# Kernel optimization log

Measured on AMD Instinct MI355X. Metric: run time of the kernel, lower is better.

Reference implementation:

```python
import jax, jax.numpy as jnp
import numpy as np

B, N, H = 8192, 8, 1024  # batch, DOF, hidden width; state dim = 2*N


def setup_inputs() -> dict:
    key = jax.random.key(0)
    ks = jax.random.split(key, 4)
    s1 = 1.0 / np.sqrt(2 * N)
    s2 = 1.0 / np.sqrt(H)
    return {
        "x": jax.random.normal(ks[0], (B, 2 * N), dtype=jnp.float32),
        "W1": jax.random.normal(ks[1], (2 * N, H), dtype=jnp.float32) * s1,
        "b1": jnp.zeros((H,), dtype=jnp.float32),
        "W2": jax.random.normal(ks[2], (H, H), dtype=jnp.float32) * s2,
        "b2": jnp.zeros((H,), dtype=jnp.float32),
        "W3": jax.random.normal(ks[3], (H, 1), dtype=jnp.float32) * s2,
        "b3": jnp.zeros((1,), dtype=jnp.float32),
    }


def reference(x, W1, b1, W2, b2, W3, b3):
    def lagrangian(q, qd):
        z = jnp.concatenate([q, qd])           # (2N,)
        h = jax.nn.softplus(z @ W1 + b1)
        h = jax.nn.softplus(h @ W2 + b2)
        return (h @ W3 + b3).sum()             # scalar L(q, qd)

    dL_dq_fn = jax.grad(lagrangian, argnums=0)
    dL_dqd_fn = jax.grad(lagrangian, argnums=1)
    # forward-over-reverse Hessian blocks (cheap: only N tangents)
    H_qdqd_fn = jax.jacfwd(dL_dqd_fn, argnums=1)   # d2L/dqd dqd, (N,N)
    H_qddq_fn = jax.jacfwd(dL_dqd_fn, argnums=0)   # d2L/dqd dq,  (N,N)

    def step(xi):
        q, qd = xi[:N], xi[N:]
        dL_dq = dL_dq_fn(q, qd)                      # (N,)
        M = H_qdqd_fn(q, qd)                         # mass-matrix block
        C = H_qddq_fn(q, qd)
        qdd = jnp.linalg.inv(M) @ (dL_dq - C @ qd)   # (N,)
        return jnp.concatenate([qd, qdd])            # (2N,)

    return jax.vmap(step)(x)
```

## Files before the change

kernel.cpp:

```cpp
#include <hip/hip_runtime.h>
#include <math.h>

#define B_ 8192
#define H_ 1024
#define LDP0 136
#define LDT 148
#define ASTR 40
#define BSTR 40

typedef short bfrag __attribute__((ext_vector_type(8)));
typedef float f4v  __attribute__((ext_vector_type(4)));

union U8 { unsigned short u[8]; uint4 v; };

__device__ __forceinline__ float sigf(float x){ return 1.0f/(1.0f+__expf(-x)); }

__device__ __forceinline__ unsigned int pkhi(unsigned int u1, unsigned int u0){
  return __builtin_amdgcn_perm(u1, u0, 0x07060302u);
}

__global__ void k1_s1(const float* __restrict__ x, const float* __restrict__ W1,
                      const float* __restrict__ b1, float* __restrict__ s1o){
  __shared__ float xs[16];
  int b = blockIdx.x, t = threadIdx.x;
  if(t < 16) xs[t] = x[b*16 + t];
  __syncthreads();
  for(int h = t; h < H_; h += 256){
    float acc = b1[h];
    #pragma unroll
    for(int j=0;j<16;j++) acc += xs[j]*W1[j*H_ + h];
    s1o[(size_t)b*H_ + h] = sigf(acc);
  }
}

__global__ __launch_bounds__(256,3) void k2_s2(const float* __restrict__ s1,
                      const float* __restrict__ W2, const float* __restrict__ b2,
                      float* __restrict__ s2o){
  __shared__ __align__(16) float As[32*LDP0];
  __shared__ __align__(16) float Bs[32*LDP0];
  int t = threadIdx.x, tx = t & 15, ty = t >> 4;
  int m0 = blockIdx.x * 128, n0 = blockIdx.y * 128;
  int jj = t & 31, rb4 = (t >> 5) * 4;
  float acc[8][8];
  #pragma unroll
  for(int i=0;i<8;i++){
    #pragma unroll
    for(int k=0;k<8;k++) acc[i][k]=0.f; }

  for(int jt=0; jt<32; jt++){
    int j0 = jt*32;
    __syncthreads();
    #pragma unroll
    for(int g=0; g<4; g++){
      #pragma unroll
      for(int i=0;i<4;i++){
        int r = rb4 + i + 32*g;
        As[jj*LDP0 + r] = -__logf(1.0f - s1[(size_t)(m0+r)*H_ + j0 + jj]);
      }
    }
    { int jB = t >> 3, kb = (t & 7) * 16;
      const float* src = &W2[(size_t)(j0 + jB)*H_ + n0 + kb];
      #pragma unroll
      for(int c=0;c<4;c++) *(float4*)&Bs[jB*LDP0 + kb + 4*c] = *(const float4*)(src + 4*c);
    }
    __syncthreads();
    #pragma unroll 8
    for(int j=0;j<32;j++){
      float4 a0 = *(const float4*)&As[j*LDP0 + 8*ty];
      float4 a1f= *(const float4*)&As[j*LDP0 + 8*ty+4];
      float4 b0 = *(const float4*)&Bs[j*LDP0 + 4*tx];
      float4 b1f= *(const float4*)&Bs[j*LDP0 + 64 + 4*tx];
      float aa[8] = {a0.x,a0.y,a0.z,a0.w,a1f.x,a1f.y,a1f.z,a1f.w};
      float bb[8] = {b0.x,b0.y,b0.z,b0.w,b1f.x,b1f.y,b1f.z,b1f.w};
      #pragma unroll
      for(int i=0;i<8;i++){
        #pragma unroll
        for(int k=0;k<8;k++) acc[i][k] += aa[i]*bb[k]; }
    }
  }
  float4 bb0 = *(const float4*)&b2[n0 + 4*tx];
  float4 bb1 = *(const float4*)&b2[n0 + 64 + 4*tx];
  #pragma unroll
  for(int i=0;i<8;i++){
    size_t r = (size_t)(m0 + 8*ty + i)*H_;
    float4 o0 = make_float4(sigf(acc[i][0]+bb0.x), sigf(acc[i][1]+bb0.y),
                            sigf(acc[i][2]+bb0.z), sigf(acc[i][3]+bb0.w));
    float4 o1 = make_float4(sigf(acc[i][4]+bb1.x), sigf(acc[i][5]+bb1.y),
                            sigf(acc[i][6]+bb1.z), sigf(acc[i][7]+bb1.w));
    *(float4*)&s2o[r + n0 + 4*tx] = o0;
    *(float4*)&s2o[r + n0 + 64 + 4*tx] = o1;
  }
}

__global__ __launch_bounds__(256,3) void k3_u(const float* __restrict__ s2,
                      const float* __restrict__ W2, const float* __restrict__ W3,
                      float* __restrict__ u){
  __shared__ __align__(16) float As[32*LDP0];
  __shared__ __align__(16) float Bs[32*LDP0];
  int t = threadIdx.x, tx = t & 15, ty = t >> 4;
  int m0 = blockIdx.x * 128, n0 = blockIdx.y * 128;
  int jj = t & 31, rb4 = (t >> 5) * 4;
  float acc[8][8];
  #pragma unroll
  for(int i=0;i<8;i++){
    #pragma unroll
    for(int k=0;k<8;k++) acc[i][k]=0.f; }

  for(int kt=0; kt<32; kt++){
    int k0 = kt*32;
    __syncthreads();
    float w3v = W3[k0 + jj];
    #pragma unroll
    for(int g=0; g<4; g++){
      #pragma unroll
      for(int i=0;i<4;i++){
        int r = rb4 + i + 32*g;
        As[jj*LDP0 + r] = w3v * s2[(size_t)(m0+r)*H_ + k0 + jj];
      }
    }
    { int jcol = t >> 1, kb = (t & 1) * 16;
      const float* src = &W2[(size_t)(n0 + jcol)*H_ + k0 + kb];
      #pragma unroll
      for(int c=0;c<16;c++) Bs[(kb+c)*LDP0 + jcol] = src[c];
    }
    __syncthreads();
    #pragma unroll 8
    for(int j=0;j<32;j++){
      float4 a0 = *(const float4*)&As[j*LDP0 + 8*ty];
      float4 a1f= *(const float4*)&As[j*LDP0 + 8*ty+4];
      float4 b0 = *(const float4*)&Bs[j*LDP0 + 4*tx];
      float4 b1f= *(const float4*)&Bs[j*LDP0 + 64 + 4*tx];
      float aa[8] = {a0.x,a0.y,a0.z,a0.w,a1f.x,a1f.y,a1f.z,a1f.w};
      float bb[8] = {b0.x,b0.y,b0.z,b0.w,b1f.x,b1f.y,b1f.z,b1f.w};
      #pragma unroll
      for(int i=0;i<8;i++){
        #pragma unroll
        for(int k=0;k<8;k++) acc[i][k] += aa[i]*bb[k]; }
    }
  }
  #pragma unroll
  for(int i=0;i<8;i++){
    size_t r = (size_t)(m0 + 8*ty + i)*H_;
    *(float4*)&u[r + n0 + 4*tx]      = make_float4(acc[i][0],acc[i][1],acc[i][2],acc[i][3]);
    *(float4*)&u[r + n0 + 64 + 4*tx] = make_float4(acc[i][4],acc[i][5],acc[i][6],acc[i][7]);
  }
}

__global__ void kF(const float* __restrict__ W1, float* __restrict__ F64){
  int e = blockIdx.x*256 + threadIdx.x;
  int j = e >> 6, p = e & 63;
  F64[e] = W1[(8+(p>>3))*H_ + j] * W1[(8+(p&7))*H_ + j];
}

__global__ __launch_bounds__(256) void k5a(const float* __restrict__ s1,
                      const float* __restrict__ u, const float* __restrict__ F64,
                      float* __restrict__ Hz1M){
  __shared__ __align__(16) float As[32*72];
  __shared__ __align__(16) float Bs[32*72];
  int t = threadIdx.x, tx = t & 15, ty = t >> 4;
  int m0 = blockIdx.x * 64;
  int jj = t & 31, rb8 = (t >> 5) * 8;
  float acc[4][4];
  #pragma unroll
  for(int i=0;i<4;i++){
    #pragma unroll
    for(int k=0;k<4;k++) acc[i][k]=0.f; }

  for(int jt=0; jt<32; jt++){
    int j0 = jt*32;
    __syncthreads();
    #pragma unroll
    for(int g=0; g<8; g++){
      int r = rb8 + g;
      float s = s1[(size_t)(m0+r)*H_ + j0 + jj];
      As[jj*72 + r] = s*(1.0f-s)*u[(size_t)(m0+r)*H_ + j0 + jj];
    }
    { int jB = t >> 3, cb = (t & 7) * 8;
      const float* src = &F64[(j0 + jB)*64 + cb];
      *(float4*)&Bs[jB*72 + cb]   = *(const float4*)(src);
      *(float4*)&Bs[jB*72 + cb+4] = *(const float4*)(src+4);
    }
    __syncthreads();
    #pragma unroll 8
    for(int j=0;j<32;j++){
      float4 a4 = *(const float4*)&As[j*72 + 4*ty];
      float4 b4 = *(const float4*)&Bs[j*72 + 4*tx];
      float aa[4] = {a4.x,a4.y,a4.z,a4.w};
      float bb[4] = {b4.x,b4.y,b4.z,b4.w};
      #pragma unroll
      for(int i=0;i<4;i++){
        #pragma unroll
        for(int k=0;k<4;k++) acc[i][k] += aa[i]*bb[k]; }
    }
  }
  #pragma unroll
  for(int i=0;i<4;i++)
    *(float4*)&Hz1M[(size_t)(m0+4*ty+i)*64 + 4*tx] =
      make_float4(acc[i][0],acc[i][1],acc[i][2],acc[i][3]);
}

__global__ void k5b(const float* __restrict__ s1, const float* __restrict__ u,
                    const float* __restrict__ W1, const float* __restrict__ x,
                    float* __restrict__ dq16){
  int wid = threadIdx.x >> 6, lane = threadIdx.x & 63;
  int b = blockIdx.x*4 + wid;
  float qd[8];
  #pragma unroll
  for(int i=0;i<8;i++) qd[i] = x[b*16 + 8 + i];
  float accd[8] = {0,0,0,0,0,0,0,0};
  float accc[8] = {0,0,0,0,0,0,0,0};
  for(int jb=0;jb<16;jb++){
    int j = jb*64 + lane;
    float s1v = s1[(size_t)b*H_+j], uv = u[(size_t)b*H_+j];
    float g1 = s1v*uv;
    float d1 = (1.0f - s1v)*g1;
    float w1q = 0.f;
    #pragma unroll
    for(int i=0;i<8;i++){ float w = W1[i*H_+j]; accd[i] += g1*w; w1q += qd[i]*w; }
    float dw = d1*w1q;
    #pragma unroll
    for(int m=0;m<8;m++) accc[m] += dw * W1[(8+m)*H_+j];
  }
  #pragma unroll
  for(int i=0;i<8;i++){
    #pragma unroll
    for(int off=1; off<64; off<<=1){
      accd[i] += __shfl_xor(accd[i], off, 64);
      accc[i] += __shfl_xor(accc[i], off, 64);
    }
  }
  if(lane==0){
    #pragma unroll
    for(int i=0;i<8;i++){ dq16[b*16+i] = accd[i]; dq16[b*16+8+i] = accc[i]; }
  }
}

__global__ void kW2T(const float* __restrict__ W2, unsigned short* __restrict__ Wh,
                     unsigned short* __restrict__ Wm, unsigned short* __restrict__ Wl){
  __shared__ float tile[32][132];
  int j0 = blockIdx.x * 32, k0 = blockIdx.y * 128;
  int t = threadIdx.x;
  int lr = t >> 3, lc0 = (t & 7) * 16;
  const float* src = &W2[(size_t)(j0+lr)*H_ + k0 + lc0];
  #pragma unroll
  for(int c=0;c<16;c+=4) *(float4*)&tile[lr][lc0+c] = *(const float4*)(src + c);
  __syncthreads();
  int k = t >> 1;
  #pragma unroll
  for(int o2=0;o2<2;o2++){
    int oc = (t&1)*2 + o2;
    U8 uh, um2, ul2;
    #pragma unroll
    for(int e=0;e<8;e++){
      float a = tile[oc*8+e][k];
      unsigned int ua = __float_as_uint(a);
      unsigned int h = ua & 0xFFFF0000u;
      float r1 = a - __uint_as_float(h);
      unsigned int m = __float_as_uint(r1) & 0xFFFF0000u;
      float l = r1 - __uint_as_float(m);
      uh.u[e]  = (unsigned short)(h >> 16);
      um2.u[e] = (unsigned short)(m >> 16);
      ul2.u[e] = (unsigned short)(__float_as_uint(l) >> 16);
    }
    size_t o = (size_t)(k0+k)*H_ + j0 + oc*8;
    *(uint4*)&Wh[o] = uh.v; *(uint4*)&Wm[o] = um2.v; *(uint4*)&Wl[o] = ul2.v;
  }
}

__global__ __launch_bounds__(256,2) void k4_mfma(
    const float* __restrict__ s1, const float* __restrict__ s2,
    const float* __restrict__ x,  const float* __restrict__ W1,
    const unsigned short* __restrict__ W2Th, const unsigned short* __restrict__ W2Tm,
    const unsigned short* __restrict__ W2Tl,
    const float* __restrict__ W3, float* __restrict__ Mpart){
  __shared__ union {
    struct { unsigned short A[3][144*ASTR]; unsigned short Bt[3][128*BSTR]; } st;
    float Td[64*LDT];
  } sm;
  __shared__ float qds[16][8];

  int t = threadIdx.x;
  int wv = t >> 6, lane = t & 63;
  int kb = blockIdx.x & 7, sgp = blockIdx.x >> 3;
  int b0 = sgp*16, k0 = kb*128;

  if(t < 128){ int s = t>>3, i = t&7; qds[s][i] = x[(b0+s)*16 + 8+i]; }

  f4v acc[9][2];
  #pragma unroll
  for(int mt=0;mt<9;mt++){
    #pragma unroll
    for(int n2=0;n2<2;n2++){ acc[mt][n2][0]=0.f; acc[mt][n2][1]=0.f; acc[mt][n2][2]=0.f; acc[mt][n2][3]=0.f; }
  }

  int aoct = t & 3, arow = t >> 2;
  int bn = t >> 1;
  int fr_m = lane & 15, fr_q = lane >> 4;

  for(int jt=0; jt<32; jt++){
    int j0 = jt*32;
    __syncthreads();
    #pragma unroll
    for(int pass=0; pass<3; pass++){
      int r = pass*64 + arow;
      if(r < 144){
        float4 w0, w1v, sa, sb;
        if(r < 128){
          int s = r>>3, m = r&7;
          const float* wp = &W1[(size_t)(8+m)*H_ + j0 + aoct*8];
          w0 = *(const float4*)wp; w1v = *(const float4*)(wp+4);
          const float* sp = &s1[(size_t)(b0+s)*H_ + j0 + aoct*8];
          sa = *(const float4*)sp; sb = *(const float4*)(sp+4);
        } else {
          int s = r - 128;
          float g0=0,g1=0,g2=0,g3=0,g4=0,g5=0,g6=0,g7=0;
          #pragma unroll
          for(int i=0;i<8;i++){
            float q = qds[s][i];
            const float* wp = &W1[(size_t)i*H_ + j0 + aoct*8];
            float4 a0 = *(const float4*)wp, a1 = *(const float4*)(wp+4);
            g0 += q*a0.x; g1 += q*a0.y; g2 += q*a0.z; g3 += q*a0.w;
            g4 += q*a1.x; g5 += q*a1.y; g6 += q*a1.z; g7 += q*a1.w;
          }
          w0 = make_float4(g0,g1,g2,g3); w1v = make_float4(g4,g5,g6,g7);
          const float* sp = &s1[(size_t)(b0+s)*H_ + j0 + aoct*8];
          sa = *(const float4*)sp; sb = *(const float4*)(sp+4);
        }
        float av[8];
        av[0]=w0.x*sa.x; av[1]=w0.y*sa.y; av[2]=w0.z*sa.z; av[3]=w0.w*sa.w;
        av[4]=w1v.x*sb.x; av[5]=w1v.y*sb.y; av[6]=w1v.z*sb.z; av[7]=w1v.w*sb.w;
        unsigned int uh[8], um[8], ul[8];
        #pragma unroll
        for(int e=0;e<8;e++){
          unsigned int ua = __float_as_uint(av[e]);
          unsigned int h = ua & 0xFFFF0000u;
          float r1 = av[e] - __uint_as_float(h);
          unsigned int m = __float_as_uint(r1) & 0xFFFF0000u;
          float l = r1 - __uint_as_float(m);
          uh[e]=h; um[e]=m; ul[e]=__float_as_uint(l);
        }
        int o = r*ASTR + aoct*8;
        uint4 vh = make_uint4(pkhi(uh[1],uh[0]), pkhi(uh[3],uh[2]), pkhi(uh[5],uh[4]), pkhi(uh[7],uh[6]));
        uint4 vm = make_uint4(pkhi(um[1],um[0]), pkhi(um[3],um[2]), pkhi(um[5],um[4]), pkhi(um[7],um[6]));
        uint4 vl = make_uint4(pkhi(ul[1],ul[0]), pkhi(ul[3],ul[2]), pkhi(ul[5],ul[4]), pkhi(ul[7],ul[6]));
        *(uint4*)&sm.st.A[0][o] = vh;
        *(uint4*)&sm.st.A[1][o] = vm;
        *(uint4*)&sm.st.A[2][o] = vl;
      }
    }
    #pragma unroll
    for(int o2=0;o2<2;o2++){
      int oc = (t&1)*2 + o2;
      size_t gsrc = (size_t)(k0+bn)*H_ + j0 + oc*8;
      int o = bn*BSTR + oc*8;
      *(uint4*)&sm.st.Bt[0][o] = *(const uint4*)&W2Th[gsrc];
      *(uint4*)&sm.st.Bt[1][o] = *(const uint4*)&W2Tm[gsrc];
      *(uint4*)&sm.st.Bt[2][o] = *(const uint4*)&W2Tl[gsrc];
    }
    __syncthreads();
    bfrag bf[2][3];
    #pragma unroll
    for(int n2=0;n2<2;n2++){
      int n = (2*wv+n2)*16 + fr_m;
      #pragma unroll
      for(int p=0;p<3;p++) bf[n2][p] = *(bfrag*)&sm.st.Bt[p][n*BSTR + fr_q*8];
    }
    #pragma unroll
    for(int mt=0; mt<9; mt++){
      int rr = mt*16 + fr_m;
      bfrag a0 = *(bfrag*)&sm.st.A[0][rr*ASTR + fr_q*8];
      bfrag a1v= *(bfrag*)&sm.st.A[1][rr*ASTR + fr_q*8];
      bfrag a2v= *(bfrag*)&sm.st.A[2][rr*ASTR + fr_q*8];
      #pragma unroll
      for(int n2=0;n2<2;n2++){
        f4v c = acc[mt][n2];
        c = __builtin_amdgcn_mfma_f32_16x16x32_bf16(a2v, bf[n2][1], c, 0,0,0);
        c = __builtin_amdgcn_mfma_f32_16x16x32_bf16(a1v, bf[n2][2], c, 0,0,0);
        c = __builtin_amdgcn_mfma_f32_16x16x32_bf16(a2v, bf[n2][0], c, 0,0,0);
        c = __builtin_amdgcn_mfma_f32_16x16x32_bf16(a0,  bf[n2][2], c, 0,0,0);
        c = __builtin_amdgcn_mfma_f32_16x16x32_bf16(a1v, bf[n2][1], c, 0,0,0);
        c = __builtin_amdgcn_mfma_f32_16x16x32_bf16(a1v, bf[n2][0], c, 0,0,0);
        c = __builtin_amdgcn_mfma_f32_16x16x32_bf16(a0,  bf[n2][1], c, 0,0,0);
        c = __builtin_amdgcn_mfma_f32_16x16x32_bf16(a0,  bf[n2][0], c, 0,0,0);
        acc[mt][n2] = c;
      }
    }
  }

  float Mp[44];
  #pragma unroll
  for(int i=0;i<44;i++) Mp[i]=0.f;
  int es = t>>4, ec = t&15;
  const float* s2p = &s2[(size_t)(b0+es)*H_ + k0];

  #pragma unroll
  for(int ph=0; ph<2; ph++){
    __syncthreads();
    if((wv>>1) == ph){
      int w1b = wv & 1;
      #pragma unroll
      for(int mt=0; mt<9; mt++){
        #pragma unroll
        for(int n2=0;n2<2;n2++){
          int col = (2*w1b+n2)*16 + fr_m;
          int rowb = mt*16 + fr_q*4;
          #pragma unroll
          for(int rg=0;rg<4;rg++)
            sm.Td[col*LDT + rowb + rg] = acc[mt][n2][rg];
        }
      }
    }
    __syncthreads();
    float4 s2v = *(const float4*)&s2p[ph*64 + ec*4];
    float4 w3v = *(const float4*)&W3[k0 + ph*64 + ec*4];
    float dv[4] = { w3v.x*s2v.x*(1.f-s2v.x), w3v.y*s2v.y*(1.f-s2v.y),
                    w3v.z*s2v.z*(1.f-s2v.z), w3v.w*s2v.w*(1.f-s2v.w) };
    #pragma unroll
    for(int e=0;e<4;e++){
      int col = ec*4+e;
      const float* tp = &sm.Td[col*LDT + es*8];
      float4 t0 = *(const float4*)tp, t1 = *(const float4*)(tp+4);
      float T8[8] = {t0.x,t0.y,t0.z,t0.w,t1.x,t1.y,t1.z,t1.w};
      float vv = sm.Td[col*LDT + 128 + es];
      float d = dv[e];
      int ix=0;
      #pragma unroll
      for(int m=0;m<8;m++){
        float w = T8[m]*d;
        Mp[36+m] += w*vv;
        #pragma unroll
        for(int n=m;n<8;n++){ Mp[ix] += w*T8[n]; ix++; }
      }
    }
  }
  #pragma unroll
  for(int i=0;i<44;i++){
    #pragma unroll
    for(int off=1; off<16; off<<=1) Mp[i] += __shfl_xor(Mp[i], off, 64);
  }
  if(ec==0){
    float* o = &Mpart[((size_t)(b0+es)*8 + kb)*44];
    #pragma unroll
    for(int i=0;i<44;i++) o[i] = Mp[i];
  }
}

__global__ __launch_bounds__(64) void k6(const float* __restrict__ x,
                    const float* __restrict__ Hz1M, const float* __restrict__ Mpart,
                    const float* __restrict__ dq16, float* __restrict__ out){
  __shared__ double A[64][73];
  int t = threadIdx.x;
  int b = blockIdx.x*64 + t;
  double* Ar = A[t];
  float qd[8];
  #pragma unroll
  for(int j=0;j<8;j++) qd[j] = x[b*16 + 8 + j];
  float Ms[44];
  #pragma unroll
  for(int i=0;i<44;i++) Ms[i]=0.f;
  for(int kb=0;kb<8;kb++){
    const float* mp = &Mpart[((size_t)b*8+kb)*44];
    #pragma unroll
    for(int i=0;i<44;i++) Ms[i] += mp[i];
  }
  #pragma unroll
  for(int i=0;i<8;i++){
    #pragma unroll
    for(int j=0;j<8;j++) Ar[i*9+j] = (double)Hz1M[(size_t)b*64 + i*8 + j];
    Ar[i*9+8] = (double)dq16[b*16+i] - (double)dq16[b*16+8+i] - (double)Ms[36+i];
  }
  { int ix=0;
    for(int m=0;m<8;m++)
      for(int n=m;n<8;n++){
        Ar[m*9+n] += (double)Ms[ix];
        if(n>m) Ar[n*9+m] += (double)Ms[ix];
        ix++;
      }
  }
  for(int c=0;c<8;c++){
    int piv = c; double best = fabs(Ar[c*9+c]);
    for(int rr=c+1; rr<8; rr++){ double v = fabs(Ar[rr*9+c]); if(v>best){best=v;piv=rr;} }
    if(piv!=c){
      for(int cc=c; cc<9; cc++){ double tmp=Ar[c*9+cc]; Ar[c*9+cc]=Ar[piv*9+cc]; Ar[piv*9+cc]=tmp; }
    }
    double inv = 1.0/Ar[c*9+c];
    for(int rr=c+1; rr<8; rr++){
      double f = Ar[rr*9+c]*inv;
      for(int cc=c+1; cc<9; cc++) Ar[rr*9+cc] -= f*Ar[c*9+cc];
    }
  }
  double sol[8];
  #pragma unroll
  for(int i=7;i>=0;i--){
    double s = Ar[i*9+8];
    #pragma unroll
    for(int j=i+1;j<8;j++) s -= Ar[i*9+j]*sol[j];
    sol[i] = s/Ar[i*9+i];
  }
  #pragma unroll
  for(int j=0;j<8;j++) out[b*16+j] = qd[j];
  #pragma unroll
  for(int i=0;i<8;i++) out[b*16+8+i] = (float)sol[i];
}

extern "C" void kernel_launch(void* const* d_in, const int* in_sizes, int n_in,
                              void* d_out, int out_size, void* d_ws, size_t ws_size,
                              hipStream_t stream){
  const float* x  = (const float*)d_in[0];
  const float* W1 = (const float*)d_in[1];
  const float* b1 = (const float*)d_in[2];
  const float* W2 = (const float*)d_in[3];
  const float* b2 = (const float*)d_in[4];
  const float* W3 = (const float*)d_in[5];
  float* out = (float*)d_out;

  float* ws   = (float*)d_ws;
  size_t BH   = (size_t)B_*H_;
  float* s1   = ws;
  float* s2   = s1  + BH;
  float* u    = s2  + BH;
  float* F64  = u   + BH;
  float* Hz1M = F64 + (size_t)H_*64;
  float* dq16 = Hz1M+ (size_t)B_*64;

  float* Mpart = u;
  unsigned short* W2Th = (unsigned short*)(u + 3145728);
  unsigned short* W2Tm = W2Th + (size_t)H_*H_;
  unsigned short* W2Tl = W2Tm + (size_t)H_*H_;

  k1_s1 <<<dim3(B_),      dim3(256), 0, stream>>>(x, W1, b1, s1);
  k2_s2 <<<dim3(64,8),    dim3(256), 0, stream>>>(s1, W2, b2, s2);
  k3_u  <<<dim3(64,8),    dim3(256), 0, stream>>>(s2, W2, W3, u);
  kF    <<<dim3(256),     dim3(256), 0, stream>>>(W1, F64);
  k5a   <<<dim3(128),     dim3(256), 0, stream>>>(s1, u, F64, Hz1M);
  k5b   <<<dim3(2048),    dim3(256), 0, stream>>>(s1, u, W1, x, dq16);
  kW2T  <<<dim3(32,8),    dim3(256), 0, stream>>>(W2, W2Th, W2Tm, W2Tl);
  k4_mfma<<<dim3(4096),   dim3(256), 0, stream>>>(s1, s2, x, W1, W2Th, W2Tm, W2Tl, W3, Mpart);
  k6    <<<dim3(128),     dim3(64),  0, stream>>>(x, Hz1M, Mpart, dq16, out);
}
```

Baseline: 2.178 ms.

## Retile k4 MFMA kernel to 8 samples per block with 64-wide K steps

The k4_mfma kernel now handles 8 batch samples per block instead of 16, so the A tile is 72 rows (padded to 80 with zeros) rather than 144, and the grid doubles to 8192 blocks. The K loop steps 64 columns at a time over 16 iterations instead of 32 columns over 32, which halves the barrier count and holds A fragments in registers across both N subtiles. The intent is to cut accumulator registers (5x2 instead of 9x2) and waste in the padded 144-row tile, in exchange for loading the W2 B tile twice as often across blocks. The LDS stride padding is removed (stride 64), which may introduce bank conflicts.

```diff
diff --git a/kernel.cpp b/kernel.cpp
--- a/kernel.cpp
+++ b/kernel.cpp
@@ -4,9 +4,7 @@
 #define B_ 8192
 #define H_ 1024
 #define LDP0 136
-#define LDT 148
-#define ASTR 40
-#define BSTR 40
+#define LDTD 100
 
 typedef short bfrag __attribute__((ext_vector_type(8)));
 typedef float f4v  __attribute__((ext_vector_type(4)));
@@ -274,115 +272,140 @@
     const unsigned short* __restrict__ W2Tl,
     const float* __restrict__ W3, float* __restrict__ Mpart){
   __shared__ union {
-    struct { unsigned short A[3][144*ASTR]; unsigned short Bt[3][128*BSTR]; } st;
-    float Td[64*LDT];
+    struct { unsigned short A[3][80*64]; unsigned short Bt[3][128*64]; } st;
+    float Td[64*LDTD];
   } sm;
-  __shared__ float qds[16][8];
+  __shared__ float qds[8][8];
 
   int t = threadIdx.x;
   int wv = t >> 6, lane = t & 63;
   int kb = blockIdx.x & 7, sgp = blockIdx.x >> 3;
-  int b0 = sgp*16, k0 = kb*128;
-
-  if(t < 128){ int s = t>>3, i = t&7; qds[s][i] = x[(b0+s)*16 + 8+i]; }
-
-  f4v acc[9][2];
-  #pragma unroll
-  for(int mt=0;mt<9;mt++){
+  int b0 = sgp*8, k0 = kb*128;
+
+  if(t < 64){ qds[t>>3][t&7] = x[(b0+(t>>3))*16 + 8 + (t&7)]; }
+  if(t < 96){
+    int p = t>>5, i16 = (t&31)*16;
+    *(uint4*)&sm.st.A[p][72*64 + i16]     = make_uint4(0,0,0,0);
+    *(uint4*)&sm.st.A[p][72*64 + i16 + 8] = make_uint4(0,0,0,0);
+  }
+
+  f4v acc[5][2];
+  #pragma unroll
+  for(int mt=0;mt<5;mt++){
     #pragma unroll
     for(int n2=0;n2<2;n2++){ acc[mt][n2][0]=0.f; acc[mt][n2][1]=0.f; acc[mt][n2][2]=0.f; acc[mt][n2][3]=0.f; }
   }
 
-  int aoct = t & 3, arow = t >> 2;
-  int bn = t >> 1;
   int fr_m = lane & 15, fr_q = lane >> 4;
-
-  for(int jt=0; jt<32; jt++){
-    int j0 = jt*32;
-    __syncthreads();
-    #pragma unroll
-    for(int pass=0; pass<3; pass++){
-      int r = pass*64 + arow;
-      if(r < 144){
-        float4 w0, w1v, sa, sb;
-        if(r < 128){
-          int s = r>>3, m = r&7;
-          const float* wp = &W1[(size_t)(8+m)*H_ + j0 + aoct*8];
-          w0 = *(const float4*)wp; w1v = *(const float4*)(wp+4);
-          const float* sp = &s1[(size_t)(b0+s)*H_ + j0 + aoct*8];
-          sa = *(const float4*)sp; sb = *(const float4*)(sp+4);
-        } else {
-          int s = r - 128;
-          float g0=0,g1=0,g2=0,g3=0,g4=0,g5=0,g6=0,g7=0;
-          #pragma unroll
-          for(int i=0;i<8;i++){
-            float q = qds[s][i];
-            const float* wp = &W1[(size_t)i*H_ + j0 + aoct*8];
-            float4 a0 = *(const float4*)wp, a1 = *(const float4*)(wp+4);
-            g0 += q*a0.x; g1 += q*a0.y; g2 += q*a0.z; g3 += q*a0.w;
-            g4 += q*a1.x; g5 += q*a1.y; g6 += q*a1.z; g7 += q*a1.w;
-          }
-          w0 = make_float4(g0,g1,g2,g3); w1v = make_float4(g4,g5,g6,g7);
-          const float* sp = &s1[(size_t)(b0+s)*H_ + j0 + aoct*8];
-          sa = *(const float4*)sp; sb = *(const float4*)(sp+4);
+  int to = t & 7, tr = t >> 3;
+  int bn = t >> 1, bh2 = t & 1;
+
+  for(int jt=0; jt<16; jt++){
+    int j0 = jt*64;
+    __syncthreads();
+    #pragma unroll
+    for(int g=0; g<2; g++){
+      int rr = tr + g*32;
+      int s = rr>>3, m = rr&7;
+      const float* wp = &W1[(size_t)(8+m)*H_ + j0 + to*8];
+      const float* sp = &s1[(size_t)(b0+s)*H_ + j0 + to*8];
+      float4 w0 = *(const float4*)wp, w1v = *(const float4*)(wp+4);
+      float4 sa = *(const float4*)sp, sb = *(const float4*)(sp+4);
+      float av[8];
+      av[0]=w0.x*sa.x; av[1]=w0.y*sa.y; av[2]=w0.z*sa.z; av[3]=w0.w*sa.w;
+      av[4]=w1v.x*sb.x; av[5]=w1v.y*sb.y; av[6]=w1v.z*sb.z; av[7]=w1v.w*sb.w;
+      unsigned int uh[8], um[8], ul[8];
+      #pragma unroll
+      for(int e=0;e<8;e++){
+        unsigned int ua = __float_as_uint(av[e]);
+        unsigned int h = ua & 0xFFFF0000u;
+        float r1 = av[e] - __uint_as_float(h);
+        unsigned int mm = __float_as_uint(r1) & 0xFFFF0000u;
+        float l = r1 - __uint_as_float(mm);
+        uh[e]=h; um[e]=mm; ul[e]=__float_as_uint(l);
+      }
+      int o = rr*64 + to*8;
+      *(uint4*)&sm.st.A[0][o] = make_uint4(pkhi(uh[1],uh[0]), pkhi(uh[3],uh[2]), pkhi(uh[5],uh[4]), pkhi(uh[7],uh[6]));
+      *(uint4*)&sm.st.A[1][o] = make_uint4(pkhi(um[1],um[0]), pkhi(um[3],um[2]), pkhi(um[5],um[4]), pkhi(um[7],um[6]));
+      *(uint4*)&sm.st.A[2][o] = make_uint4(pkhi(ul[1],ul[0]), pkhi(ul[3],ul[2]), pkhi(ul[5],ul[4]), pkhi(ul[7],ul[6]));
+    }
+    if(t < 64){
+      int s = tr;
+      float g8[8] = {0,0,0,0,0,0,0,0};
+      #pragma unroll
+      for(int i=0;i<8;i++){
+        float q = qds[s][i];
+        const float* wp = &W1[(size_t)i*H_ + j0 + to*8];
+        float4 a0 = *(const float4*)wp, a1 = *(const float4*)(wp+4);
+        g8[0] += q*a0.x; g8[1] += q*a0.y; g8[2] += q*a0.z; g8[3] += q*a0.w;
+        g8[4] += q*a1.x; g8[5] += q*a1.y; g8[6] += q*a1.z; g8[7] += q*a1.w;
+      }
+      const float* sp = &s1[(size_t)(b0+s)*H_ + j0 + to*8];
+      float4 sa = *(const float4*)sp, sb = *(const float4*)(sp+4);
+      float av[8];
+      av[0]=g8[0]*sa.x; av[1]=g8[1]*sa.y; av[2]=g8[2]*sa.z; av[3]=g8[3]*sa.w;
+      av[4]=g8[4]*sb.x; av[5]=g8[5]*sb.y; av[6]=g8[6]*sb.z; av[7]=g8[7]*sb.w;
+      unsigned int uh[8], um[8], ul[8];
+      #pragma unroll
+      for(int e=0;e<8;e++){
+        unsigned int ua = __float_as_uint(av[e]);
+        unsigned int h = ua & 0xFFFF0000u;
+        float r1 = av[e] - __uint_as_float(h);
+        unsigned int mm = __float_as_uint(r1) & 0xFFFF0000u;
+        float l = r1 - __uint_as_float(mm);
+        uh[e]=h; um[e]=mm; ul[e]=__float_as_uint(l);
+      }
+      int o = (64+s)*64 + to*8;
+      *(uint4*)&sm.st.A[0][o] = make_uint4(pkhi(uh[1],uh[0]), pkhi(uh[3],uh[2]), pkhi(uh[5],uh[4]), pkhi(uh[7],uh[6]));
+      *(uint4*)&sm.st.A[1][o] = make_uint4(pkhi(um[1],um[0]), pkhi(um[3],um[2]), pkhi(um[5],um[4]), pkhi(um[7],um[6]));
+      *(uint4*)&sm.st.A[2][o] = make_uint4(pkhi(ul[1],ul[0]), pkhi(ul[3],ul[2]), pkhi(ul[5],ul[4]), pkhi(ul[7],ul[6]));
+    }
+    {
+      size_t gsrc = (size_t)(k0+bn)*H_ + j0 + bh2*32;
+      int o = bn*64 + bh2*32;
+      *(uint4*)&sm.st.Bt[0][o]    = *(const uint4*)&W2Th[gsrc];
+      *(uint4*)&sm.st.Bt[0][o+8]  = *(const uint4*)&W2Th[gsrc+8];
+      *(uint4*)&sm.st.Bt[0][o+16] = *(const uint4*)&W2Th[gsrc+16];
+      *(uint4*)&sm.st.Bt[0][o+24] = *(const uint4*)&W2Th[gsrc+24];
+      *(uint4*)&sm.st.Bt[1][o]    = *(const uint4*)&W2Tm[gsrc];
+      *(uint4*)&sm.st.Bt[1][o+8]  = *(const uint4*)&W2Tm[gsrc+8];
+      *(uint4*)&sm.st.Bt[1][o+16] = *(const uint4*)&W2Tm[gsrc+16];
+      *(uint4*)&sm.st.Bt[1][o+24] = *(const uint4*)&W2Tm[gsrc+24];
+      *(uint4*)&sm.st.Bt[2][o]    = *(const uint4*)&W2Tl[gsrc];
+      *(uint4*)&sm.st.Bt[2][o+8]  = *(const uint4*)&W2Tl[gsrc+8];
+      *(uint4*)&sm.st.Bt[2][o+16] = *(const uint4*)&W2Tl[gsrc+16];
+      *(uint4*)&sm.st.Bt[2][o+24] = *(const uint4*)&W2Tl[gsrc+24];
+    }
+    __syncthreads();
+    #pragma unroll
+    for(int ks=0; ks<2; ks++){
+      bfrag af[5][3];
+      #pragma unroll
+      for(int mt=0; mt<5; mt++){
+        int ao = (mt*16 + fr_m)*64 + ks*32 + fr_q*8;
+        af[mt][0] = *(bfrag*)&sm.st.A[0][ao];
+        af[mt][1] = *(bfrag*)&sm.st.A[1][ao];
+        af[mt][2] = *(bfrag*)&sm.st.A[2][ao];
+      }
+      #pragma unroll
+      for(int n2=0;n2<2;n2++){
+        int bo = ((2*wv+n2)*16 + fr_m)*64 + ks*32 + fr_q*8;
+        bfrag bhf = *(bfrag*)&sm.st.Bt[0][bo];
+        bfrag bmf = *(bfrag*)&sm.st.Bt[1][bo];
+        bfrag blf = *(bfrag*)&sm.st.Bt[2][bo];
+        #pragma unroll
+        for(int mt=0; mt<5; mt++){
+          f4v c = acc[mt][n2];
+          c = __builtin_amdgcn_mfma_f32_16x16x32_bf16(af[mt][2], bmf, c, 0,0,0);
+          c = __builtin_amdgcn_mfma_f32_16x16x32_bf16(af[mt][1], blf, c, 0,0,0);
+          c = __builtin_amdgcn_mfma_f32_16x16x32_bf16(af[mt][2], bhf, c, 0,0,0);
+          c = __builtin_amdgcn_mfma_f32_16x16x32_bf16(af[mt][0], blf, c, 0,0,0);
+          c = __builtin_amdgcn_mfma_f32_16x16x32_bf16(af[mt][1], bmf, c, 0,0,0);
+          c = __builtin_amdgcn_mfma_f32_16x16x32_bf16(af[mt][1], bhf, c, 0,0,0);
+          c = __builtin_amdgcn_mfma_f32_16x16x32_bf16(af[mt][0], bmf, c, 0,0,0);
+          c = __builtin_amdgcn_mfma_f32_16x16x32_bf16(af[mt][0], bhf, c, 0,0,0);
+          acc[mt][n2] = c;
         }
-        float av[8];
-        av[0]=w0.x*sa.x; av[1]=w0.y*sa.y; av[2]=w0.z*sa.z; av[3]=w0.w*sa.w;
-        av[4]=w1v.x*sb.x; av[5]=w1v.y*sb.y; av[6]=w1v.z*sb.z; av[7]=w1v.w*sb.w;
-        unsigned int uh[8], um[8], ul[8];
-        #pragma unroll
-        for(int e=0;e<8;e++){
-          unsigned int ua = __float_as_uint(av[e]);
-          unsigned int h = ua & 0xFFFF0000u;
-          float r1 = av[e] - __uint_as_float(h);
-          unsigned int m = __float_as_uint(r1) & 0xFFFF0000u;
-          float l = r1 - __uint_as_float(m);
-          uh[e]=h; um[e]=m; ul[e]=__float_as_uint(l);
-        }
-        int o = r*ASTR + aoct*8;
-        uint4 vh = make_uint4(pkhi(uh[1],uh[0]), pkhi(uh[3],uh[2]), pkhi(uh[5],uh[4]), pkhi(uh[7],uh[6]));
-        uint4 vm = make_uint4(pkhi(um[1],um[0]), pkhi(um[3],um[2]), pkhi(um[5],um[4]), pkhi(um[7],um[6]));
-        uint4 vl = make_uint4(pkhi(ul[1],ul[0]), pkhi(ul[3],ul[2]), pkhi(ul[5],ul[4]), pkhi(ul[7],ul[6]));
-        *(uint4*)&sm.st.A[0][o] = vh;
-        *(uint4*)&sm.st.A[1][o] = vm;
-        *(uint4*)&sm.st.A[2][o] = vl;
-      }
-    }
-    #pragma unroll
-    for(int o2=0;o2<2;o2++){
-      int oc = (t&1)*2 + o2;
-      size_t gsrc = (size_t)(k0+bn)*H_ + j0 + oc*8;
-      int o = bn*BSTR + oc*8;
-      *(uint4*)&sm.st.Bt[0][o] = *(const uint4*)&W2Th[gsrc];
-      *(uint4*)&sm.st.Bt[1][o] = *(const uint4*)&W2Tm[gsrc];
-      *(uint4*)&sm.st.Bt[2][o] = *(const uint4*)&W2Tl[gsrc];
-    }
-    __syncthreads();
-    bfrag bf[2][3];
-    #pragma unroll
-    for(int n2=0;n2<2;n2++){
-      int n = (2*wv+n2)*16 + fr_m;
-      #pragma unroll
-      for(int p=0;p<3;p++) bf[n2][p] = *(bfrag*)&sm.st.Bt[p][n*BSTR + fr_q*8];
-    }
-    #pragma unroll
-    for(int mt=0; mt<9; mt++){
-      int rr = mt*16 + fr_m;
-      bfrag a0 = *(bfrag*)&sm.st.A[0][rr*ASTR + fr_q*8];
-      bfrag a1v= *(bfrag*)&sm.st.A[1][rr*ASTR + fr_q*8];
-      bfrag a2v= *(bfrag*)&sm.st.A[2][rr*ASTR + fr_q*8];
-      #pragma unroll
-      for(int n2=0;n2<2;n2++){
-        f4v c = acc[mt][n2];
-        c = __builtin_amdgcn_mfma_f32_16x16x32_bf16(a2v, bf[n2][1], c, 0,0,0);
-        c = __builtin_amdgcn_mfma_f32_16x16x32_bf16(a1v, bf[n2][2], c, 0,0,0);
-        c = __builtin_amdgcn_mfma_f32_16x16x32_bf16(a2v, bf[n2][0], c, 0,0,0);
-        c = __builtin_amdgcn_mfma_f32_16x16x32_bf16(a0,  bf[n2][2], c, 0,0,0);
-        c = __builtin_amdgcn_mfma_f32_16x16x32_bf16(a1v, bf[n2][1], c, 0,0,0);
-        c = __builtin_amdgcn_mfma_f32_16x16x32_bf16(a1v, bf[n2][0], c, 0,0,0);
-        c = __builtin_amdgcn_mfma_f32_16x16x32_bf16(a0,  bf[n2][1], c, 0,0,0);
-        c = __builtin_amdgcn_mfma_f32_16x16x32_bf16(a0,  bf[n2][0], c, 0,0,0);
-        acc[mt][n2] = c;
       }
     }
   }
@@ -390,39 +413,37 @@
   float Mp[44];
   #pragma unroll
   for(int i=0;i<44;i++) Mp[i]=0.f;
-  int es = t>>4, ec = t&15;
-  const float* s2p = &s2[(size_t)(b0+es)*H_ + k0];
+  int es = t>>5, ec = t&31;
 
   #pragma unroll
   for(int ph=0; ph<2; ph++){
     __syncthreads();
     if((wv>>1) == ph){
-      int w1b = wv & 1;
-      #pragma unroll
-      for(int mt=0; mt<9; mt++){
+      int wb = wv & 1;
+      #pragma unroll
+      for(int mt=0; mt<5; mt++){
         #pragma unroll
         for(int n2=0;n2<2;n2++){
-          int col = (2*w1b+n2)*16 + fr_m;
+          int col = (2*wb+n2)*16 + fr_m;
           int rowb = mt*16 + fr_q*4;
           #pragma unroll
           for(int rg=0;rg<4;rg++)
-            sm.Td[col*LDT + rowb + rg] = acc[mt][n2][rg];
+            sm.Td[col*LDTD + rowb + rg] = acc[mt][n2][rg];
         }
       }
     }
     __syncthreads();
-    float4 s2v = *(const float4*)&s2p[ph*64 + ec*4];
-    float4 w3v = *(const float4*)&W3[k0 + ph*64 + ec*4];
-    float dv[4] = { w3v.x*s2v.x*(1.f-s2v.x), w3v.y*s2v.y*(1.f-s2v.y),
-                    w3v.z*s2v.z*(1.f-s2v.z), w3v.w*s2v.w*(1.f-s2v.w) };
-    #pragma unroll
-    for(int e=0;e<4;e++){
-      int col = ec*4+e;
-      const float* tp = &sm.Td[col*LDT + es*8];
+    #pragma unroll
+    for(int cc=0; cc<2; cc++){
+      int col = ec + cc*32;
+      int kk = ph*64 + col;
+      float s2v = s2[(size_t)(b0+es)*H_ + k0 + kk];
+      float w3v = W3[k0 + kk];
+      float d = w3v*s2v*(1.f-s2v);
+      const float* tp = &sm.Td[col*LDTD + es*8];
       float4 t0 = *(const float4*)tp, t1 = *(const float4*)(tp+4);
       float T8[8] = {t0.x,t0.y,t0.z,t0.w,t1.x,t1.y,t1.z,t1.w};
-      float vv = sm.Td[col*LDT + 128 + es];
-      float d = dv[e];
+      float vv = sm.Td[col*LDTD + 64 + es];
       int ix=0;
       #pragma unroll
       for(int m=0;m<8;m++){
@@ -436,7 +457,7 @@
   #pragma unroll
   for(int i=0;i<44;i++){
     #pragma unroll
-    for(int off=1; off<16; off<<=1) Mp[i] += __shfl_xor(Mp[i], off, 64);
+    for(int off=1; off<32; off<<=1) Mp[i] += __shfl_xor(Mp[i], off, 64);
   }
   if(ec==0){
     float* o = &Mpart[((size_t)(b0+es)*8 + kb)*44];
@@ -535,6 +556,6 @@
   k5a   <<<dim3(128),     dim3(256), 0, stream>>>(s1, u, F64, Hz1M);
   k5b   <<<dim3(2048),    dim3(256), 0, stream>>>(s1, u, W1, x, dq16);
   kW2T  <<<dim3(32,8),    dim3(256), 0, stream>>>(W2, W2Th, W2Tm, W2Tl);
-  k4_mfma<<<dim3(4096),   dim3(256), 0, stream>>>(s1, s2, x, W1, W2Th, W2Tm, W2Tl, W3, Mpart);
+  k4_mfma<<<dim3(8192),   dim3(256), 0, stream>>>(s1, s2, x, W1, W2Th, W2Tm, W2Tl, W3, Mpart);
   k6    <<<dim3(128),     dim3(64),  0, stream>>>(x, Hz1M, Mpart, dq16, out);
 }
```

Result: slower. 6.042 ms (+177.3%).
